# Performance work log

Hardware: AMD Instinct MI355X
Metric: run time of the kernel (lower is better)

The kernel has to match this reference:

```python
import jax, jax.numpy as jnp
import numpy as np

EPS = 1e-5
GROUPS = 384

def _dwconv(x, w, stride, pad):
    # x: [N,C,H,W], w: [O, C/groups, kh, kw] (depthwise: C/groups == 1)
    return jax.lax.conv_general_dilated(
        x, w,
        window_strides=(stride, stride),
        padding=[(pad, pad), (pad, pad)],
        dimension_numbers=('NCHW', 'OIHW', 'NCHW'),
        feature_group_count=GROUPS,
    )

def _bn(y, gamma, beta):
    # training-mode BatchNorm2d: batch statistics over (N,H,W)
    mean = jnp.mean(y, axis=(0, 2, 3), keepdims=True)
    var = jnp.var(y, axis=(0, 2, 3), keepdims=True)
    g = gamma[None, :, None, None]
    b = beta[None, :, None, None]
    return (y - mean) * jax.lax.rsqrt(var + EPS) * g + b

def setup_inputs() -> dict:
    key = jax.random.key(0)
    k1, k2, k3 = jax.random.split(key, 3)
    C = 384
    x = jax.random.normal(k1, (32, C, 64, 64), dtype=jnp.float32)
    w_lk = jax.random.normal(k2, (C, 1, 7, 7), dtype=jnp.float32) * 0.05
    w_sk = jax.random.normal(k3, (C, 1, 3, 3), dtype=jnp.float32) * 0.1
    gamma_lk = jnp.ones((C,), jnp.float32)
    beta_lk = jnp.zeros((C,), jnp.float32)
    gamma_sk = jnp.ones((C,), jnp.float32)
    beta_sk = jnp.zeros((C,), jnp.float32)
    return {"x": x, "w_lk": w_lk, "gamma_lk": gamma_lk, "beta_lk": beta_lk,
            "w_sk": w_sk, "gamma_sk": gamma_sk, "beta_sk": beta_sk}

def reference(x, w_lk, gamma_lk, beta_lk, w_sk, gamma_sk, beta_sk):
    stride = 2
    # large-kernel depthwise branch: conv7x7 (pad 3) + BN
    out = _bn(_dwconv(x, w_lk, stride, 3), gamma_lk, beta_lk)
    # small-kernel depthwise branch: conv3x3 (pad 1) + BN, added in
    out = out + _bn(_dwconv(x, w_sk, stride, 1), gamma_sk, beta_sk)
    # exact (erf) GELU, matching torch nn.GELU() default
    return jax.nn.gelu(out, approximate=False)
```

## Files before the change

kernel.cpp:

```cpp
#include <hip/hip_runtime.h>
#include <hip/hip_fp16.h>
#include <cmath>

#define NB 32
#define CH 384
#define IH 64
#define IW 64
#define OH 32
#define OW 32
#define PR 69
#define SF 18

typedef unsigned int u32x4 __attribute__((ext_vector_type(4)));
typedef float        f32x4 __attribute__((ext_vector_type(4)));

__global__ __launch_bounds__(128, 4) void conv_stats_kernel(
    const float* __restrict__ x,
    const float* __restrict__ w_lk,
    const float* __restrict__ w_sk,
    uint2* __restrict__ yls,
    float* __restrict__ partial)
{
    __shared__ float4 sxf[PR][SF];

    const int nc  = blockIdx.x;
    const int n   = nc / CH;
    const int c   = nc % CH;
    const int tid = threadIdx.x;

    const float4* xp4 = (const float4*)(x + (size_t)nc * (IH * IW));
    float4 vbuf[8];
#pragma unroll
    for (int it = 0; it < 8; ++it) vbuf[it] = xp4[tid + it * 128];

    const float4 z4 = make_float4(0.f, 0.f, 0.f, 0.f);

    for (int i = tid; i < 5 * SF; i += 128) {
        const int r = i / SF, q = i % SF;
        sxf[(r < 3) ? r : (r + 64)][q] = z4;
    }
    {
        const int i = tid;
        const int r = 3 + (i >> 1);
        sxf[r][(i & 1) ? 17 : 0] = z4;
    }

#pragma unroll
    for (int it = 0; it < 8; ++it) {
        const int i = tid + it * 128;
        const int r  = (i >> 4) + 3;
        const int q4 = i & 15;
        sxf[r][q4 + 1] = vbuf[it];
    }
    __syncthreads();

    float wl[49], ws9[9];
#pragma unroll
    for (int t = 0; t < 49; ++t) wl[t] = w_lk[c * 49 + t];
#pragma unroll
    for (int t = 0; t < 9; ++t)  ws9[t] = w_sk[c * 9 + t];

    const int lane = tid & 63;
    const int wv   = tid >> 6;
    const int j16  = lane & 15;
    const int g    = lane >> 4;
    const int oy0  = (wv * 4 + g) * 4;
    const int prb  = 2 * oy0;

    float alA[4] = {0.f,0.f,0.f,0.f}, alB[4] = {0.f,0.f,0.f,0.f};
    float asA[4] = {0.f,0.f,0.f,0.f}, asB[4] = {0.f,0.f,0.f,0.f};

#pragma unroll
    for (int k = 0; k < 13; ++k) {
        const int pr = prb + k;
        const float4 X0 = sxf[pr][j16];
        const float4 X1 = sxf[pr][j16 + 1];
        const float4 X2 = sxf[pr][j16 + 2];
#pragma unroll
        for (int j = 0; j < 4; ++j) {
            if (k >= 2 * j && k <= 2 * j + 6) {
                const int ky = k - 2 * j;
                alA[j] = fmaf(X0.y, wl[ky * 7 + 0], alA[j]);
                alA[j] = fmaf(X0.z, wl[ky * 7 + 1], alA[j]);
                alA[j] = fmaf(X0.w, wl[ky * 7 + 2], alA[j]);
                alA[j] = fmaf(X1.x, wl[ky * 7 + 3], alA[j]);
                alA[j] = fmaf(X1.y, wl[ky * 7 + 4], alA[j]);
                alA[j] = fmaf(X1.z, wl[ky * 7 + 5], alA[j]);
                alA[j] = fmaf(X1.w, wl[ky * 7 + 6], alA[j]);
                alB[j] = fmaf(X0.w, wl[ky * 7 + 0], alB[j]);
                alB[j] = fmaf(X1.x, wl[ky * 7 + 1], alB[j]);
                alB[j] = fmaf(X1.y, wl[ky * 7 + 2], alB[j]);
                alB[j] = fmaf(X1.z, wl[ky * 7 + 3], alB[j]);
                alB[j] = fmaf(X1.w, wl[ky * 7 + 4], alB[j]);
                alB[j] = fmaf(X2.x, wl[ky * 7 + 5], alB[j]);
                alB[j] = fmaf(X2.y, wl[ky * 7 + 6], alB[j]);
            }
            if (k >= 2 * j + 2 && k <= 2 * j + 4) {
                const int ks = k - 2 * j - 2;
                asA[j] = fmaf(X0.w, ws9[ks * 3 + 0], asA[j]);
                asA[j] = fmaf(X1.x, ws9[ks * 3 + 1], asA[j]);
                asA[j] = fmaf(X1.y, ws9[ks * 3 + 2], asA[j]);
                asB[j] = fmaf(X1.y, ws9[ks * 3 + 0], asB[j]);
                asB[j] = fmaf(X1.z, ws9[ks * 3 + 1], asB[j]);
                asB[j] = fmaf(X1.w, ws9[ks * 3 + 2], asB[j]);
            }
        }
    }

    float s0 = 0.f, s1 = 0.f, s2 = 0.f, s3 = 0.f;
    uint2* yp = yls + (size_t)nc * (OH * OW / 2);
#pragma unroll
    for (int j = 0; j < 4; ++j) {
        const int oy = oy0 + j;
        const __half2 hA = __floats2half2_rn(alA[j], asA[j]);
        const __half2 hB = __floats2half2_rn(alB[j], asB[j]);
        uint2 u;
        u.x = *reinterpret_cast<const unsigned int*>(&hA);
        u.y = *reinterpret_cast<const unsigned int*>(&hB);
        yp[oy * (OW / 2) + j16] = u;
        s0 += alA[j] + alB[j];
        s1 += alA[j] * alA[j] + alB[j] * alB[j];
        s2 += asA[j] + asB[j];
        s3 += asA[j] * asA[j] + asB[j] * asB[j];
    }

#pragma unroll
    for (int off = 32; off >= 1; off >>= 1) {
        s0 += __shfl_down(s0, off);
        s1 += __shfl_down(s1, off);
        s2 += __shfl_down(s2, off);
        s3 += __shfl_down(s3, off);
    }
    if (lane == 0) {
        ((float4*)partial)[(c * NB + n) * 2 + wv] = make_float4(s0, s1, s2, s3);
    }
}

__global__ __launch_bounds__(256) void apply_kernel(
    const u32x4* __restrict__ yls4,
    const float* __restrict__ partial,
    const float* __restrict__ gamma_lk, const float* __restrict__ beta_lk,
    const float* __restrict__ gamma_sk, const float* __restrict__ beta_sk,
    f32x4* __restrict__ out)
{
    __shared__ float sp[4];

    const int b = blockIdx.x;
    const int c = b % CH;
    const int tid = threadIdx.x;

    if (tid < 64) {
        float4 v = ((const float4*)partial)[c * 64 + tid];
        float s0 = v.x, s1 = v.y, s2 = v.z, s3 = v.w;
#pragma unroll
        for (int off = 32; off >= 1; off >>= 1) {
            s0 += __shfl_down(s0, off);
            s1 += __shfl_down(s1, off);
            s2 += __shfl_down(s2, off);
            s3 += __shfl_down(s3, off);
        }
        if (tid == 0) {
            const float inv_cnt = 1.0f / (float)(NB * OH * OW);
            const float mean_l = s0 * inv_cnt;
            const float var_l  = s1 * inv_cnt - mean_l * mean_l;
            const float sc_l   = gamma_lk[c] * rsqrtf(var_l + 1e-5f);
            const float sh_l   = beta_lk[c] - mean_l * sc_l;
            const float mean_s = s2 * inv_cnt;
            const float var_s  = s3 * inv_cnt - mean_s * mean_s;
            const float sc_s   = gamma_sk[c] * rsqrtf(var_s + 1e-5f);
            const float sh_s   = beta_sk[c] - mean_s * sc_s;
            sp[0] = sc_l; sp[1] = sh_l; sp[2] = sc_s; sp[3] = sh_s;
        }
    }
    __syncthreads();

    const float sc_l = sp[0], sh_l = sp[1], sc_s = sp[2], sh_s = sp[3];

    const int i = b * 256 + tid;
    const u32x4 v = __builtin_nontemporal_load(yls4 + i);
    const unsigned int uv0 = v.x, uv1 = v.y, uv2 = v.z, uv3 = v.w;
    const __half2 h0 = *reinterpret_cast<const __half2*>(&uv0);
    const __half2 h1 = *reinterpret_cast<const __half2*>(&uv1);
    const __half2 h2 = *reinterpret_cast<const __half2*>(&uv2);
    const __half2 h3 = *reinterpret_cast<const __half2*>(&uv3);

    const float v0 = fmaf(__low2float(h0), sc_l, sh_l) + fmaf(__high2float(h0), sc_s, sh_s);
    const float v1 = fmaf(__low2float(h1), sc_l, sh_l) + fmaf(__high2float(h1), sc_s, sh_s);
    const float v2 = fmaf(__low2float(h2), sc_l, sh_l) + fmaf(__high2float(h2), sc_s, sh_s);
    const float v3 = fmaf(__low2float(h3), sc_l, sh_l) + fmaf(__high2float(h3), sc_s, sh_s);

    f32x4 r;
    r.x = 0.5f * v0 * (1.0f + erff(v0 * 0.70710678118654752f));
    r.y = 0.5f * v1 * (1.0f + erff(v1 * 0.70710678118654752f));
    r.z = 0.5f * v2 * (1.0f + erff(v2 * 0.70710678118654752f));
    r.w = 0.5f * v3 * (1.0f + erff(v3 * 0.70710678118654752f));
    __builtin_nontemporal_store(r, out + i);
}

extern "C" void kernel_launch(void* const* d_in, const int* in_sizes, int n_in,
                              void* d_out, int out_size, void* d_ws, size_t ws_size,
                              hipStream_t stream) {
    const float* x        = (const float*)d_in[0];
    const float* w_lk     = (const float*)d_in[1];
    const float* gamma_lk = (const float*)d_in[2];
    const float* beta_lk  = (const float*)d_in[3];
    const float* w_sk     = (const float*)d_in[4];
    const float* gamma_sk = (const float*)d_in[5];
    const float* beta_sk  = (const float*)d_in[6];
    float* out = (float*)d_out;

    float* partial = (float*)d_ws;
    uint2* yls     = (uint2*)(partial + CH * NB * 2 * 4);

    conv_stats_kernel<<<NB * CH, 128, 0, stream>>>(x, w_lk, w_sk, yls, partial);
    apply_kernel<<<NB * CH, 256, 0, stream>>>(
        (const u32x4*)yls, partial, gamma_lk, beta_lk, gamma_sk, beta_sk,
        (f32x4*)out);
}
```

Before: 72.76 us.

## Stage conv input tile in shared memory as fp16 split planes

The padded input tile is now stored in LDS as __half2 values split across two planes (even and odd pairs) instead of float4, which halves shared-memory footprint and read traffic per tap. Occupancy is raised through a larger launch-bounds block minimum, which the smaller LDS allocation allows. Each tap read now needs half-to-float conversions, and rounding the input to fp16 before the convolution loses precision relative to the fp32 reference.

```diff
diff --git a/kernel.cpp b/kernel.cpp
--- a/kernel.cpp
+++ b/kernel.cpp
@@ -8,20 +8,20 @@
 #define IW 64
 #define OH 32
 #define OW 32
-#define PR 69
-#define SF 18
+#define PR 70
+#define SQ 18
 
 typedef unsigned int u32x4 __attribute__((ext_vector_type(4)));
 typedef float        f32x4 __attribute__((ext_vector_type(4)));
 
-__global__ __launch_bounds__(128, 4) void conv_stats_kernel(
+__global__ __launch_bounds__(128, 6) void conv_stats_kernel(
     const float* __restrict__ x,
     const float* __restrict__ w_lk,
     const float* __restrict__ w_sk,
     uint2* __restrict__ yls,
     float* __restrict__ partial)
 {
-    __shared__ float4 sxf[PR][SF];
+    __shared__ __half2 sx2[2][PR][SQ];
 
     const int nc  = blockIdx.x;
     const int n   = nc / CH;
@@ -33,24 +33,30 @@
 #pragma unroll
     for (int it = 0; it < 8; ++it) vbuf[it] = xp4[tid + it * 128];
 
-    const float4 z4 = make_float4(0.f, 0.f, 0.f, 0.f);
-
-    for (int i = tid; i < 5 * SF; i += 128) {
-        const int r = i / SF, q = i % SF;
-        sxf[(r < 3) ? r : (r + 64)][q] = z4;
-    }
-    {
-        const int i = tid;
-        const int r = 3 + (i >> 1);
-        sxf[r][(i & 1) ? 17 : 0] = z4;
+    const __half2 z2 = __floats2half2_rn(0.f, 0.f);
+
+    for (int i = tid; i < 2 * 5 * SQ; i += 128) {
+        const int e = i / (5 * SQ);
+        const int rem = i % (5 * SQ);
+        const int r = rem / SQ, q = rem % SQ;
+        sx2[e][(r < 3) ? r : (r + 64)][q] = z2;
+    }
+    for (int i = tid; i < 64 * 3; i += 128) {
+        const int r = 3 + i / 3;
+        const int t = i % 3;
+        if (t == 0)      sx2[0][r][0]  = z2;
+        else if (t == 1) sx2[1][r][0]  = z2;
+        else             sx2[0][r][17] = z2;
     }
 
 #pragma unroll
     for (int it = 0; it < 8; ++it) {
         const int i = tid + it * 128;
+        const float4 v = vbuf[it];
         const int r  = (i >> 4) + 3;
         const int q4 = i & 15;
-        sxf[r][q4 + 1] = vbuf[it];
+        sx2[0][r][q4 + 1] = __floats2half2_rn(v.x, v.y);
+        sx2[1][r][q4 + 1] = __floats2half2_rn(v.z, v.w);
     }
     __syncthreads();
 
@@ -73,36 +79,47 @@
 #pragma unroll
     for (int k = 0; k < 13; ++k) {
         const int pr = prb + k;
-        const float4 X0 = sxf[pr][j16];
-        const float4 X1 = sxf[pr][j16 + 1];
-        const float4 X2 = sxf[pr][j16 + 2];
+        const __half2 P0 = sx2[0][pr][j16];
+        const __half2 P1 = sx2[1][pr][j16];
+        const __half2 P2 = sx2[0][pr][j16 + 1];
+        const __half2 P3 = sx2[1][pr][j16 + 1];
+        const __half2 P4 = sx2[0][pr][j16 + 2];
+        const float c1 = __high2float(P0);
+        const float c2 = __low2float(P1);
+        const float c3 = __high2float(P1);
+        const float c4 = __low2float(P2);
+        const float c5 = __high2float(P2);
+        const float c6 = __low2float(P3);
+        const float c7 = __high2float(P3);
+        const float c8 = __low2float(P4);
+        const float c9 = __high2float(P4);
 #pragma unroll
         for (int j = 0; j < 4; ++j) {
             if (k >= 2 * j && k <= 2 * j + 6) {
                 const int ky = k - 2 * j;
-                alA[j] = fmaf(X0.y, wl[ky * 7 + 0], alA[j]);
-                alA[j] = fmaf(X0.z, wl[ky * 7 + 1], alA[j]);
-                alA[j] = fmaf(X0.w, wl[ky * 7 + 2], alA[j]);
-                alA[j] = fmaf(X1.x, wl[ky * 7 + 3], alA[j]);
-                alA[j] = fmaf(X1.y, wl[ky * 7 + 4], alA[j]);
-                alA[j] = fmaf(X1.z, wl[ky * 7 + 5], alA[j]);
-                alA[j] = fmaf(X1.w, wl[ky * 7 + 6], alA[j]);
-                alB[j] = fmaf(X0.w, wl[ky * 7 + 0], alB[j]);
-                alB[j] = fmaf(X1.x, wl[ky * 7 + 1], alB[j]);
-                alB[j] = fmaf(X1.y, wl[ky * 7 + 2], alB[j]);
-                alB[j] = fmaf(X1.z, wl[ky * 7 + 3], alB[j]);
-                alB[j] = fmaf(X1.w, wl[ky * 7 + 4], alB[j]);
-                alB[j] = fmaf(X2.x, wl[ky * 7 + 5], alB[j]);
-                alB[j] = fmaf(X2.y, wl[ky * 7 + 6], alB[j]);
+                alA[j] = fmaf(c1, wl[ky * 7 + 0], alA[j]);
+                alA[j] = fmaf(c2, wl[ky * 7 + 1], alA[j]);
+                alA[j] = fmaf(c3, wl[ky * 7 + 2], alA[j]);
+                alA[j] = fmaf(c4, wl[ky * 7 + 3], alA[j]);
+                alA[j] = fmaf(c5, wl[ky * 7 + 4], alA[j]);
+                alA[j] = fmaf(c6, wl[ky * 7 + 5], alA[j]);
+                alA[j] = fmaf(c7, wl[ky * 7 + 6], alA[j]);
+                alB[j] = fmaf(c3, wl[ky * 7 + 0], alB[j]);
+                alB[j] = fmaf(c4, wl[ky * 7 + 1], alB[j]);
+                alB[j] = fmaf(c5, wl[ky * 7 + 2], alB[j]);
+                alB[j] = fmaf(c6, wl[ky * 7 + 3], alB[j]);
+                alB[j] = fmaf(c7, wl[ky * 7 + 4], alB[j]);
+                alB[j] = fmaf(c8, wl[ky * 7 + 5], alB[j]);
+                alB[j] = fmaf(c9, wl[ky * 7 + 6], alB[j]);
             }
             if (k >= 2 * j + 2 && k <= 2 * j + 4) {
                 const int ks = k - 2 * j - 2;
-                asA[j] = fmaf(X0.w, ws9[ks * 3 + 0], asA[j]);
-                asA[j] = fmaf(X1.x, ws9[ks * 3 + 1], asA[j]);
-                asA[j] = fmaf(X1.y, ws9[ks * 3 + 2], asA[j]);
-                asB[j] = fmaf(X1.y, ws9[ks * 3 + 0], asB[j]);
-                asB[j] = fmaf(X1.z, ws9[ks * 3 + 1], asB[j]);
-                asB[j] = fmaf(X1.w, ws9[ks * 3 + 2], asB[j]);
+                asA[j] = fmaf(c3, ws9[ks * 3 + 0], asA[j]);
+                asA[j] = fmaf(c4, ws9[ks * 3 + 1], asA[j]);
+                asA[j] = fmaf(c5, ws9[ks * 3 + 2], asA[j]);
+                asB[j] = fmaf(c5, ws9[ks * 3 + 0], asB[j]);
+                asB[j] = fmaf(c6, ws9[ks * 3 + 1], asB[j]);
+                asB[j] = fmaf(c7, ws9[ks * 3 + 2], asB[j]);
             }
         }
     }
```

Result: faster. 64.44 us (-11.4%).
